# Optimization experiments

Measured on AMD Instinct MI355X. Metric: run time of the kernel, lower is better.

## Reference

```python
import jax, jax.numpy as jnp
import numpy as np

EPS = 0.01       # perturbation radius (constructor arg)
MEAN = 0.1307    # MNIST normalize constants from the 'else' branch
SIGMA = 0.3081


def _get_bound(v, eps):
    # torch get_bound detaches eps before taking |.| and summing
    r = jnp.sum(jnp.abs(jax.lax.stop_gradient(eps)), axis=-1)
    return v + r, v - r


def _relu_zono(v, eps):
    # v: [N], eps: [N, E]. Append one fresh (zero) error column, as the torch code does.
    n = v.shape[0]
    eps = jnp.concatenate([eps, jnp.zeros((n, 1), eps.dtype)], axis=-1)  # [N, E+1]
    u, l = _get_bound(v, eps)
    denom = u - l  # = 2*sum|eps| >= 0; guard against 0 for non-crossing rows
    # slopes are created as Parameters = u/(u-l) on the first pass (detached leaf)
    slope = jax.lax.stop_gradient(u / jnp.where(denom == 0, 1.0, denom))
    # at init slope == base = u/(u-l), so the slope <= base branch is taken
    term = (1.0 - slope) * u * 0.5
    crossing = (u > 0) & (l < 0)
    dead = u <= 0
    # torch uses slope.data * values.data for the linear part, + term (term carries grad)
    v_cross = jax.lax.stop_gradient(slope * v) + term
    v_new = jnp.where(dead, 0.0, jnp.where(crossing, v_cross, v))
    eps_cross = jnp.concatenate([slope[:, None] * eps[:, :-1], term[:, None]], axis=-1)
    eps_new = jnp.where(dead[:, None], 0.0, jnp.where(crossing[:, None], eps_cross, eps))
    return v_new, eps_new


def _forward(inputs, W1, b1, W2, b2, W3, b3):
    # initial zonotope build (faithful to source: values = u + l, radii = values - l = u)
    upper = jnp.minimum(inputs + EPS, 1.0)   # upper - relu(upper - 1)
    lower = jnp.maximum(inputs - EPS, 0.0)   # relu(lower)
    values = upper + lower
    eps = jnp.diag((values - lower).flatten())  # [D, D]
    # Normalize layer (the 'else' branch)
    values = (values - MEAN) / SIGMA
    eps = eps / SIGMA
    # Flatten
    v = values.flatten()
    # Linear -> ReLU -> Linear -> ReLU -> Linear
    v = W1 @ v + b1
    eps = W1 @ eps
    v, eps = _relu_zono(v, eps)
    v = W2 @ v + b2
    eps = W2 @ eps
    v, eps = _relu_zono(v, eps)
    v = W3 @ v + b3
    eps = W3 @ eps
    u, l = _get_bound(v, eps)
    return u, l


def setup_inputs() -> dict:
    key = jax.random.key(0)
    ks = jax.random.split(key, 7)
    D, H, O = 1024, 4096, 10
    inputs = jax.random.uniform(ks[0], (1, 1, 32, 32), jnp.float32)
    W1 = jax.random.normal(ks[1], (H, D), jnp.float32) / np.float32(np.sqrt(D))
    b1 = jax.random.normal(ks[2], (H,), jnp.float32) * 0.01
    W2 = jax.random.normal(ks[3], (H, H), jnp.float32) / np.float32(np.sqrt(H))
    b2 = jax.random.normal(ks[4], (H,), jnp.float32) * 0.01
    W3 = jax.random.normal(ks[5], (O, H), jnp.float32) / np.float32(np.sqrt(H))
    b3 = jax.random.normal(ks[6], (O,), jnp.float32) * 0.01
    return {"inputs": inputs, "W1": W1, "b1": b1, "W2": W2, "b2": b2, "W3": W3, "b3": b3}


def reference(inputs, W1, b1, W2, b2, W3, b3):
    return _forward(inputs, W1, b1, W2, b2, W3, b3)
```

## Files before the change

kernel.cpp:

```cpp
#include <hip/hip_runtime.h>
#include <math.h>

#define ZEPS  0.01f
#define ZMEAN 0.1307f
#define ZSIGMA 0.3081f

constexpr int D = 1024, H = 4096, O = 10;

using short8 = __attribute__((ext_vector_type(8))) short;
using f32x4  = __attribute__((ext_vector_type(4))) float;

__device__ inline unsigned short f2bf(float x) {
    unsigned int u = __float_as_uint(x);
    u += 0x7FFFu + ((u >> 16) & 1u);
    return (unsigned short)(u >> 16);
}

__device__ inline void gl_lds16(const void* g, void* l) {
    __builtin_amdgcn_global_load_lds(
        (const __attribute__((address_space(1))) unsigned int*)g,
        (__attribute__((address_space(3))) unsigned int*)l, 16, 0, 0);
}

__device__ inline void relu_params(float v, float r, float& vout, float& aout, float& tout) {
    float u = v + r, l = v - r;
    float denom = u - l;
    float slope = u / (denom == 0.f ? 1.f : denom);
    float term = (1.f - slope) * u * 0.5f;
    bool dead = (u <= 0.f);
    bool crossing = (u > 0.f) && (l < 0.f);
    vout = dead ? 0.f : (crossing ? (slope * v + term) : v);
    aout = dead ? 0.f : (crossing ? slope : 1.f);
    tout = (!dead && crossing) ? term : 0.f;
}

__global__ void k_setup(const float* __restrict__ x, float* __restrict__ values,
                        float* __restrict__ dcol, float* __restrict__ r3) {
    int j = blockIdx.x * blockDim.x + threadIdx.x;
    if (j < D) {
        float v = x[j];
        float up = fminf(v + ZEPS, 1.f);
        float lo = fmaxf(v - ZEPS, 0.f);
        values[j] = (up + lo - ZMEAN) / ZSIGMA;
        dcol[j]   = up / ZSIGMA;
    }
    if (blockIdx.x == 0 && threadIdx.x < 16) r3[threadIdx.x] = 0.f;
}

__global__ __launch_bounds__(256) void k_layer1(const float* __restrict__ W1, const float* __restrict__ b1,
                                                const float* __restrict__ values, const float* __restrict__ dcol,
                                                float* __restrict__ v1p, float* __restrict__ a1,
                                                float* __restrict__ t1) {
    int i = blockIdx.x, tid = threadIdx.x;
    const float* row = W1 + (size_t)i * D;
    float sv = 0.f, sr = 0.f;
    for (int j = tid; j < D; j += 256) {
        float w = row[j];
        sv += w * values[j];
        sr += fabsf(w) * dcol[j];
    }
    __shared__ float red1[256], red2[256];
    red1[tid] = sv; red2[tid] = sr;
    __syncthreads();
    for (int off = 128; off; off >>= 1) {
        if (tid < off) { red1[tid] += red1[tid + off]; red2[tid] += red2[tid + off]; }
        __syncthreads();
    }
    if (tid == 0) {
        float v = red1[0] + b1[i];
        relu_params(v, red2[0], v1p[i], a1[i], t1[i]);
    }
}

__global__ __launch_bounds__(256) void k_scaleT(const float* __restrict__ W1, const float* __restrict__ a1,
                                                const float* __restrict__ dcol,
                                                unsigned short* __restrict__ W1sT) {
    __shared__ float tile[32][33];
    int j0 = blockIdx.x * 32, k0 = blockIdx.y * 32;
    int r = threadIdx.x >> 3;
    int c = (threadIdx.x & 7) * 4;
    float4 w = *(const float4*)&W1[(size_t)(k0 + r) * D + j0 + c];
    float a = a1[k0 + r];
    tile[r][c + 0] = a * w.x * dcol[j0 + c + 0];
    tile[r][c + 1] = a * w.y * dcol[j0 + c + 1];
    tile[r][c + 2] = a * w.z * dcol[j0 + c + 2];
    tile[r][c + 3] = a * w.w * dcol[j0 + c + 3];
    __syncthreads();
    ushort4 o;
    o.x = f2bf(tile[c + 0][r]);
    o.y = f2bf(tile[c + 1][r]);
    o.z = f2bf(tile[c + 2][r]);
    o.w = f2bf(tile[c + 3][r]);
    *(ushort4*)&W1sT[(size_t)(j0 + r) * H + k0 + c] = o;
}

__global__ __launch_bounds__(256) void k_v2conv(const float* __restrict__ W2, const float* __restrict__ b2,
                                                const float* __restrict__ v1p, const float* __restrict__ t1,
                                                float* __restrict__ v2, float* __restrict__ t2col,
                                                unsigned short* __restrict__ W2b) {
    int i = blockIdx.x, tid = threadIdx.x;
    const float* row = W2 + (size_t)i * H;
    unsigned short* orow = W2b + (size_t)i * H;
    float sv = 0.f, st = 0.f;
    for (int k0 = tid * 4; k0 < H; k0 += 1024) {
        float4 w = *(const float4*)&row[k0];
        sv += w.x * v1p[k0] + w.y * v1p[k0 + 1] + w.z * v1p[k0 + 2] + w.w * v1p[k0 + 3];
        st += w.x * t1[k0] + w.y * t1[k0 + 1] + w.z * t1[k0 + 2] + w.w * t1[k0 + 3];
        ushort4 o;
        o.x = f2bf(w.x); o.y = f2bf(w.y); o.z = f2bf(w.z); o.w = f2bf(w.w);
        *(ushort4*)&orow[k0] = o;
    }
    __shared__ float red1[256], red2[256];
    red1[tid] = sv; red2[tid] = st;
    __syncthreads();
    for (int off = 128; off; off >>= 1) {
        if (tid < off) { red1[tid] += red1[tid + off]; red2[tid] += red2[tid + off]; }
        __syncthreads();
    }
    if (tid == 0) { v2[i] = red1[0] + b2[i]; t2col[i] = red2[0]; }
}

#define GBK 64
__global__ __launch_bounds__(256) void k_gemm_mfma(const unsigned short* __restrict__ A,
                                                   const unsigned short* __restrict__ B,
                                                   float* __restrict__ C) {
    const int N = D, K = H;
    __shared__ __align__(16) unsigned short As[128 * GBK];
    __shared__ __align__(16) unsigned short Bs[128 * GBK];
    int tid = threadIdx.x;
    int wave = tid >> 6, lane = tid & 63;
    int bm = blockIdx.y * 128, bn = blockIdx.x * 128;
    int kbeg = blockIdx.z * (K / 2), kend = kbeg + K / 2;
    float* Cz = C + (size_t)blockIdx.z * ((size_t)H * D);
    int wm = (wave >> 1) * 64, wn = (wave & 1) * 64;

    int sr = lane >> 3;
    int sc = lane & 7;
    int scp = sc ^ sr;
    int r15 = lane & 15, quad = lane >> 4, key = r15 & 7;

    f32x4 acc[4][4];
#pragma unroll
    for (int p = 0; p < 4; ++p)
#pragma unroll
        for (int q = 0; q < 4; ++q) acc[p][q] = (f32x4){0.f, 0.f, 0.f, 0.f};

    for (int k0 = kbeg; k0 < kend; k0 += GBK) {
#pragma unroll
        for (int g = 0; g < 4; ++g) {
            int row = wave * 32 + g * 8;
            gl_lds16(&A[(size_t)(bm + row + sr) * K + k0 + scp * 8], &As[row * GBK]);
            gl_lds16(&B[(size_t)(bn + row + sr) * K + k0 + scp * 8], &Bs[row * GBK]);
        }
        __syncthreads();
#pragma unroll
        for (int kk = 0; kk < 2; ++kk) {
            short8 af[4], bf[4];
#pragma unroll
            for (int mt = 0; mt < 4; ++mt)
                af[mt] = *(const short8*)&As[(wm + mt * 16 + r15) * GBK + (((kk * 4 + quad) ^ key)) * 8];
#pragma unroll
            for (int nt = 0; nt < 4; ++nt)
                bf[nt] = *(const short8*)&Bs[(wn + nt * 16 + r15) * GBK + (((kk * 4 + quad) ^ key)) * 8];
#pragma unroll
            for (int mt = 0; mt < 4; ++mt)
#pragma unroll
                for (int nt = 0; nt < 4; ++nt)
                    acc[mt][nt] = __builtin_amdgcn_mfma_f32_16x16x32_bf16(af[mt], bf[nt], acc[mt][nt], 0, 0, 0);
        }
        __syncthreads();
    }

#pragma unroll
    for (int mt = 0; mt < 4; ++mt) {
        int gr = bm + wm + mt * 16 + quad * 4;
#pragma unroll
        for (int nt = 0; nt < 4; ++nt) {
            int gc = bn + wn + nt * 16 + r15;
            Cz[(size_t)(gr + 0) * N + gc] = acc[mt][nt][0];
            Cz[(size_t)(gr + 1) * N + gc] = acc[mt][nt][1];
            Cz[(size_t)(gr + 2) * N + gc] = acc[mt][nt][2];
            Cz[(size_t)(gr + 3) * N + gc] = acc[mt][nt][3];
        }
    }
}

__global__ __launch_bounds__(256) void k_relu2(const float* __restrict__ e1, const float* __restrict__ e2,
                                               const float* __restrict__ t2col,
                                               const float* __restrict__ v2, float* __restrict__ v2p,
                                               float* __restrict__ a2, float* __restrict__ t2) {
    int i = blockIdx.x, tid = threadIdx.x;
    float4 a = ((const float4*)(e1 + (size_t)i * D))[tid];
    float4 b = ((const float4*)(e2 + (size_t)i * D))[tid];
    float s = fabsf(a.x + b.x) + fabsf(a.y + b.y) + fabsf(a.z + b.z) + fabsf(a.w + b.w);
    __shared__ float red[256];
    red[tid] = s;
    __syncthreads();
    for (int off = 128; off; off >>= 1) {
        if (tid < off) red[tid] += red[tid + off];
        __syncthreads();
    }
    if (tid == 0) {
        float r = red[0] + fabsf(t2col[i]);
        relu_params(v2[i], r, v2p[i], a2[i], t2[i]);
    }
}

__global__ void k_w3s(const float* __restrict__ W3, const float* __restrict__ a2,
                      float* __restrict__ w3s) {
    int i = blockIdx.x * blockDim.x + threadIdx.x;
    if (i < H) {
        float a = a2[i];
#pragma unroll
        for (int o = 0; o < O; ++o) w3s[(size_t)i * O + o] = W3[(size_t)o * H + i] * a;
    }
}

__global__ __launch_bounds__(256) void k_eps3a(const float* __restrict__ e1, const float* __restrict__ e2,
                                               const float* __restrict__ w3s,
                                               float* __restrict__ pbuf) {
    int jb = blockIdx.x, ib = blockIdx.y;
    int c = threadIdx.x & 63, s = threadIdx.x >> 6;
    int j = jb * 64 + c;
    int i0 = ib * 128 + s * 32;
    float acc[O];
#pragma unroll
    for (int o = 0; o < O; ++o) acc[o] = 0.f;
    for (int ii = 0; ii < 32; ++ii) {
        int i = i0 + ii;
        float e = e1[(size_t)i * D + j] + e2[(size_t)i * D + j];
        const float* w = &w3s[(size_t)i * O];
#pragma unroll
        for (int o = 0; o < O; ++o) acc[o] += w[o] * e;
    }
    __shared__ float sm[4][64][O];
#pragma unroll
    for (int o = 0; o < O; ++o) sm[s][c][o] = acc[o];
    __syncthreads();
    for (int idx = threadIdx.x; idx < 64 * O; idx += 256) {
        int o = idx >> 6, cc = idx & 63;
        float t = sm[0][cc][o] + sm[1][cc][o] + sm[2][cc][o] + sm[3][cc][o];
        pbuf[((size_t)ib * O + o) * D + jb * 64 + cc] = t;
    }
}

__global__ __launch_bounds__(256) void k_eps3b(const float* __restrict__ pbuf, float* __restrict__ r3) {
    int o = blockIdx.x, tid = threadIdx.x;
    float s = 0.f;
    for (int j = tid; j < D; j += 256) {
        float t = 0.f;
#pragma unroll
        for (int ib = 0; ib < 32; ++ib) t += pbuf[((size_t)ib * O + o) * D + j];
        s += fabsf(t);
    }
    __shared__ float red[256];
    red[tid] = s;
    __syncthreads();
    for (int off = 128; off; off >>= 1) {
        if (tid < off) red[tid] += red[tid + off];
        __syncthreads();
    }
    if (tid == 0) r3[o] = red[0];
}

__global__ __launch_bounds__(256) void k_final(const float* __restrict__ W3, const float* __restrict__ b3,
                                               const float* __restrict__ v2p, const float* __restrict__ a2,
                                               const float* __restrict__ t2col, const float* __restrict__ t2,
                                               const float* __restrict__ r3, float* __restrict__ out) {
    int o = blockIdx.x, tid = threadIdx.x;
    const float* row = W3 + (size_t)o * H;
    float sv = 0.f, s1 = 0.f, s2 = 0.f;
    for (int i = tid; i < H; i += 256) {
        float w = row[i];
        sv += w * v2p[i];
        s1 += w * a2[i] * t2col[i];
        s2 += w * t2[i];
    }
    __shared__ float ra[256], rb[256], rc[256];
    ra[tid] = sv; rb[tid] = s1; rc[tid] = s2;
    __syncthreads();
    for (int off = 128; off; off >>= 1) {
        if (tid < off) { ra[tid] += ra[tid + off]; rb[tid] += rb[tid + off]; rc[tid] += rc[tid + off]; }
        __syncthreads();
    }
    if (tid == 0) {
        float v3 = ra[0] + b3[o];
        float rr = r3[o] + fabsf(rb[0]) + fabsf(rc[0]);
        out[o] = v3 + rr;
        out[O + o] = v3 - rr;
    }
}

extern "C" void kernel_launch(void* const* d_in, const int* in_sizes, int n_in,
                              void* d_out, int out_size, void* d_ws, size_t ws_size,
                              hipStream_t stream) {
    const float* x  = (const float*)d_in[0];
    const float* W1 = (const float*)d_in[1];
    const float* b1 = (const float*)d_in[2];
    const float* W2 = (const float*)d_in[3];
    const float* b2 = (const float*)d_in[4];
    const float* W3 = (const float*)d_in[5];
    const float* b3 = (const float*)d_in[6];
    float* out = (float*)d_out;

    float* p = (float*)d_ws;
    float* values = p; p += D;
    float* dcol   = p; p += D;
    float* v1p    = p; p += H;
    float* a1     = p; p += H;
    float* t1     = p; p += H;
    float* v2     = p; p += H;
    float* t2col  = p; p += H;
    float* v2p    = p; p += H;
    float* a2     = p; p += H;
    float* t2     = p; p += H;
    float* r3     = p; p += 16;
    p += 16;
    float* w3s    = p; p += H * O + 8;
    float* pbuf   = p; p += 32 * O * D;
    float* eps2   = p; p += (size_t)2 * H * D;
    unsigned short* W2b  = (unsigned short*)p;
    unsigned short* W1sT = W2b + (size_t)H * H;
    float* eps2b = eps2 + (size_t)H * D;

    k_setup<<<dim3((D + 255) / 256), 256, 0, stream>>>(x, values, dcol, r3);
    k_layer1<<<H, 256, 0, stream>>>(W1, b1, values, dcol, v1p, a1, t1);
    k_scaleT<<<dim3(D / 32, H / 32), 256, 0, stream>>>(W1, a1, dcol, W1sT);
    k_v2conv<<<H, 256, 0, stream>>>(W2, b2, v1p, t1, v2, t2col, W2b);
    k_gemm_mfma<<<dim3(D / 128, H / 128, 2), 256, 0, stream>>>(W2b, W1sT, eps2);
    k_relu2<<<H, 256, 0, stream>>>(eps2, eps2b, t2col, v2, v2p, a2, t2);
    k_w3s<<<(H + 255) / 256, 256, 0, stream>>>(W3, a2, w3s);
    k_eps3a<<<dim3(D / 64, 32), 256, 0, stream>>>(eps2, eps2b, w3s, pbuf);
    k_eps3b<<<O, 256, 0, stream>>>(pbuf, r3);
    k_final<<<O, 256, 0, stream>>>(W3, b3, v2p, a2, t2col, t2, r3, out);
}
```

Baseline: 228.3 us.

## Fuse setup, w3s and eps3b kernels; remap GEMM blocks; vectorize eps3a

Removes three small kernels by recomputing the input transform inline in layer1/scaleT, folding the W3 scaling into relu2, and merging the final eps3 reduction into k_final. The GEMM grid is flattened to 1D with a remapping that places both K-halves and neighbouring tiles on adjacent block IDs, likely for cache locality across XCDs. k_eps3a now processes four columns per thread with float4 loads, and the pbuf layout is transposed so k_final reads it contiguously. The goal is fewer launches and better memory access, at the cost of a heavier 16-way shared reduction in eps3a and a k_final that does more serial work in only 10 blocks.

```diff
diff --git a/kernel.cpp b/kernel.cpp
--- a/kernel.cpp
+++ b/kernel.cpp
@@ -20,6 +20,15 @@
     __builtin_amdgcn_global_load_lds(
         (const __attribute__((address_space(1))) unsigned int*)g,
         (__attribute__((address_space(3))) unsigned int*)l, 16, 0, 0);
+}
+
+__device__ inline float zval(float xv) {
+    float up = fminf(xv + ZEPS, 1.f);
+    float lo = fmaxf(xv - ZEPS, 0.f);
+    return (up + lo - ZMEAN) / ZSIGMA;
+}
+__device__ inline float zdia(float xv) {
+    return fminf(xv + ZEPS, 1.f) / ZSIGMA;
 }
 
 __device__ inline void relu_params(float v, float r, float& vout, float& aout, float& tout) {
@@ -34,21 +43,8 @@
     tout = (!dead && crossing) ? term : 0.f;
 }
 
-__global__ void k_setup(const float* __restrict__ x, float* __restrict__ values,
-                        float* __restrict__ dcol, float* __restrict__ r3) {
-    int j = blockIdx.x * blockDim.x + threadIdx.x;
-    if (j < D) {
-        float v = x[j];
-        float up = fminf(v + ZEPS, 1.f);
-        float lo = fmaxf(v - ZEPS, 0.f);
-        values[j] = (up + lo - ZMEAN) / ZSIGMA;
-        dcol[j]   = up / ZSIGMA;
-    }
-    if (blockIdx.x == 0 && threadIdx.x < 16) r3[threadIdx.x] = 0.f;
-}
-
 __global__ __launch_bounds__(256) void k_layer1(const float* __restrict__ W1, const float* __restrict__ b1,
-                                                const float* __restrict__ values, const float* __restrict__ dcol,
+                                                const float* __restrict__ x,
                                                 float* __restrict__ v1p, float* __restrict__ a1,
                                                 float* __restrict__ t1) {
     int i = blockIdx.x, tid = threadIdx.x;
@@ -56,8 +52,9 @@
     float sv = 0.f, sr = 0.f;
     for (int j = tid; j < D; j += 256) {
         float w = row[j];
-        sv += w * values[j];
-        sr += fabsf(w) * dcol[j];
+        float xv = x[j];
+        sv += w * zval(xv);
+        sr += fabsf(w) * zdia(xv);
     }
     __shared__ float red1[256], red2[256];
     red1[tid] = sv; red2[tid] = sr;
@@ -73,18 +70,19 @@
 }
 
 __global__ __launch_bounds__(256) void k_scaleT(const float* __restrict__ W1, const float* __restrict__ a1,
-                                                const float* __restrict__ dcol,
+                                                const float* __restrict__ x,
                                                 unsigned short* __restrict__ W1sT) {
     __shared__ float tile[32][33];
     int j0 = blockIdx.x * 32, k0 = blockIdx.y * 32;
     int r = threadIdx.x >> 3;
     int c = (threadIdx.x & 7) * 4;
     float4 w = *(const float4*)&W1[(size_t)(k0 + r) * D + j0 + c];
+    float4 xx = *(const float4*)&x[j0 + c];
     float a = a1[k0 + r];
-    tile[r][c + 0] = a * w.x * dcol[j0 + c + 0];
-    tile[r][c + 1] = a * w.y * dcol[j0 + c + 1];
-    tile[r][c + 2] = a * w.z * dcol[j0 + c + 2];
-    tile[r][c + 3] = a * w.w * dcol[j0 + c + 3];
+    tile[r][c + 0] = a * w.x * zdia(xx.x);
+    tile[r][c + 1] = a * w.y * zdia(xx.y);
+    tile[r][c + 2] = a * w.z * zdia(xx.z);
+    tile[r][c + 3] = a * w.w * zdia(xx.w);
     __syncthreads();
     ushort4 o;
     o.x = f2bf(tile[c + 0][r]);
@@ -127,11 +125,16 @@
     const int N = D, K = H;
     __shared__ __align__(16) unsigned short As[128 * GBK];
     __shared__ __align__(16) unsigned short Bs[128 * GBK];
+    int b = blockIdx.x;
+    int u = b & 7, v = b >> 3;
+    int z = u >> 2;
+    int y = (u & 3) * 8 + (v >> 3);
+    int xb = v & 7;
     int tid = threadIdx.x;
     int wave = tid >> 6, lane = tid & 63;
-    int bm = blockIdx.y * 128, bn = blockIdx.x * 128;
-    int kbeg = blockIdx.z * (K / 2), kend = kbeg + K / 2;
-    float* Cz = C + (size_t)blockIdx.z * ((size_t)H * D);
+    int bm = y * 128, bn = xb * 128;
+    int kbeg = z * (K / 2), kend = kbeg + K / 2;
+    float* Cz = C + (size_t)z * ((size_t)H * D);
     int wm = (wave >> 1) * 64, wn = (wave & 1) * 64;
 
     int sr = lane >> 3;
@@ -187,13 +190,16 @@
 
 __global__ __launch_bounds__(256) void k_relu2(const float* __restrict__ e1, const float* __restrict__ e2,
                                                const float* __restrict__ t2col,
-                                               const float* __restrict__ v2, float* __restrict__ v2p,
-                                               float* __restrict__ a2, float* __restrict__ t2) {
+                                               const float* __restrict__ v2, const float* __restrict__ W3,
+                                               float* __restrict__ v2p,
+                                               float* __restrict__ a2, float* __restrict__ t2,
+                                               float* __restrict__ w3s) {
     int i = blockIdx.x, tid = threadIdx.x;
     float4 a = ((const float4*)(e1 + (size_t)i * D))[tid];
     float4 b = ((const float4*)(e2 + (size_t)i * D))[tid];
     float s = fabsf(a.x + b.x) + fabsf(a.y + b.y) + fabsf(a.z + b.z) + fabsf(a.w + b.w);
     __shared__ float red[256];
+    __shared__ float s_a2;
     red[tid] = s;
     __syncthreads();
     for (int off = 128; off; off >>= 1) {
@@ -202,72 +208,67 @@
     }
     if (tid == 0) {
         float r = red[0] + fabsf(t2col[i]);
-        relu_params(v2[i], r, v2p[i], a2[i], t2[i]);
-    }
-}
-
-__global__ void k_w3s(const float* __restrict__ W3, const float* __restrict__ a2,
-                      float* __restrict__ w3s) {
-    int i = blockIdx.x * blockDim.x + threadIdx.x;
-    if (i < H) {
-        float a = a2[i];
-#pragma unroll
-        for (int o = 0; o < O; ++o) w3s[(size_t)i * O + o] = W3[(size_t)o * H + i] * a;
-    }
+        float vo, ao, to;
+        relu_params(v2[i], r, vo, ao, to);
+        v2p[i] = vo; a2[i] = ao; t2[i] = to;
+        s_a2 = ao;
+    }
+    __syncthreads();
+    if (tid < O) w3s[(size_t)i * O + tid] = W3[(size_t)tid * H + i] * s_a2;
 }
 
 __global__ __launch_bounds__(256) void k_eps3a(const float* __restrict__ e1, const float* __restrict__ e2,
                                                const float* __restrict__ w3s,
                                                float* __restrict__ pbuf) {
     int jb = blockIdx.x, ib = blockIdx.y;
-    int c = threadIdx.x & 63, s = threadIdx.x >> 6;
-    int j = jb * 64 + c;
-    int i0 = ib * 128 + s * 32;
-    float acc[O];
-#pragma unroll
-    for (int o = 0; o < O; ++o) acc[o] = 0.f;
-    for (int ii = 0; ii < 32; ++ii) {
+    int jj = threadIdx.x & 15, s = threadIdx.x >> 4;
+    int j = jb * 64 + jj * 4;
+    int i0 = ib * 128 + s * 8;
+    float acc[4][O];
+#pragma unroll
+    for (int c = 0; c < 4; ++c)
+#pragma unroll
+        for (int o = 0; o < O; ++o) acc[c][o] = 0.f;
+    for (int ii = 0; ii < 8; ++ii) {
         int i = i0 + ii;
-        float e = e1[(size_t)i * D + j] + e2[(size_t)i * D + j];
+        float4 a = *(const float4*)&e1[(size_t)i * D + j];
+        float4 b = *(const float4*)&e2[(size_t)i * D + j];
+        float e0 = a.x + b.x, ee1 = a.y + b.y, ee2 = a.z + b.z, ee3 = a.w + b.w;
         const float* w = &w3s[(size_t)i * O];
 #pragma unroll
-        for (int o = 0; o < O; ++o) acc[o] += w[o] * e;
-    }
-    __shared__ float sm[4][64][O];
-#pragma unroll
-    for (int o = 0; o < O; ++o) sm[s][c][o] = acc[o];
+        for (int o = 0; o < O; ++o) {
+            float wo = w[o];
+            acc[0][o] += wo * e0; acc[1][o] += wo * ee1;
+            acc[2][o] += wo * ee2; acc[3][o] += wo * ee3;
+        }
+    }
+    __shared__ float sm[16][64][O];
+#pragma unroll
+    for (int c = 0; c < 4; ++c)
+#pragma unroll
+        for (int o = 0; o < O; ++o) sm[s][jj * 4 + c][o] = acc[c][o];
     __syncthreads();
     for (int idx = threadIdx.x; idx < 64 * O; idx += 256) {
-        int o = idx >> 6, cc = idx & 63;
-        float t = sm[0][cc][o] + sm[1][cc][o] + sm[2][cc][o] + sm[3][cc][o];
-        pbuf[((size_t)ib * O + o) * D + jb * 64 + cc] = t;
-    }
-}
-
-__global__ __launch_bounds__(256) void k_eps3b(const float* __restrict__ pbuf, float* __restrict__ r3) {
-    int o = blockIdx.x, tid = threadIdx.x;
-    float s = 0.f;
-    for (int j = tid; j < D; j += 256) {
+        int col = idx / O, o = idx % O;
         float t = 0.f;
 #pragma unroll
-        for (int ib = 0; ib < 32; ++ib) t += pbuf[((size_t)ib * O + o) * D + j];
-        s += fabsf(t);
-    }
-    __shared__ float red[256];
-    red[tid] = s;
-    __syncthreads();
-    for (int off = 128; off; off >>= 1) {
-        if (tid < off) red[tid] += red[tid + off];
-        __syncthreads();
-    }
-    if (tid == 0) r3[o] = red[0];
+        for (int ss = 0; ss < 16; ++ss) t += sm[ss][col][o];
+        pbuf[((size_t)o * 32 + ib) * D + jb * 64 + col] = t;
+    }
 }
 
 __global__ __launch_bounds__(256) void k_final(const float* __restrict__ W3, const float* __restrict__ b3,
                                                const float* __restrict__ v2p, const float* __restrict__ a2,
                                                const float* __restrict__ t2col, const float* __restrict__ t2,
-                                               const float* __restrict__ r3, float* __restrict__ out) {
+                                               const float* __restrict__ pbuf, float* __restrict__ out) {
     int o = blockIdx.x, tid = threadIdx.x;
+    float s3 = 0.f;
+    for (int j = tid; j < D; j += 256) {
+        float t = 0.f;
+#pragma unroll
+        for (int ib = 0; ib < 32; ++ib) t += pbuf[((size_t)o * 32 + ib) * D + j];
+        s3 += fabsf(t);
+    }
     const float* row = W3 + (size_t)o * H;
     float sv = 0.f, s1 = 0.f, s2 = 0.f;
     for (int i = tid; i < H; i += 256) {
@@ -276,16 +277,19 @@
         s1 += w * a2[i] * t2col[i];
         s2 += w * t2[i];
     }
-    __shared__ float ra[256], rb[256], rc[256];
-    ra[tid] = sv; rb[tid] = s1; rc[tid] = s2;
+    __shared__ float ra[256], rb[256], rc[256], rd[256];
+    ra[tid] = sv; rb[tid] = s1; rc[tid] = s2; rd[tid] = s3;
     __syncthreads();
     for (int off = 128; off; off >>= 1) {
-        if (tid < off) { ra[tid] += ra[tid + off]; rb[tid] += rb[tid + off]; rc[tid] += rc[tid + off]; }
+        if (tid < off) {
+            ra[tid] += ra[tid + off]; rb[tid] += rb[tid + off];
+            rc[tid] += rc[tid + off]; rd[tid] += rd[tid + off];
+        }
         __syncthreads();
     }
     if (tid == 0) {
         float v3 = ra[0] + b3[o];
-        float rr = r3[o] + fabsf(rb[0]) + fabsf(rc[0]);
+        float rr = rd[0] + fabsf(rb[0]) + fabsf(rc[0]);
         out[o] = v3 + rr;
         out[O + o] = v3 - rr;
     }
@@ -304,8 +308,6 @@
     float* out = (float*)d_out;
 
     float* p = (float*)d_ws;
-    float* values = p; p += D;
-    float* dcol   = p; p += D;
     float* v1p    = p; p += H;
     float* a1     = p; p += H;
     float* t1     = p; p += H;
@@ -314,8 +316,6 @@
     float* v2p    = p; p += H;
     float* a2     = p; p += H;
     float* t2     = p; p += H;
-    float* r3     = p; p += 16;
-    p += 16;
     float* w3s    = p; p += H * O + 8;
     float* pbuf   = p; p += 32 * O * D;
     float* eps2   = p; p += (size_t)2 * H * D;
@@ -323,14 +323,11 @@
     unsigned short* W1sT = W2b + (size_t)H * H;
     float* eps2b = eps2 + (size_t)H * D;
 
-    k_setup<<<dim3((D + 255) / 256), 256, 0, stream>>>(x, values, dcol, r3);
-    k_layer1<<<H, 256, 0, stream>>>(W1, b1, values, dcol, v1p, a1, t1);
-    k_scaleT<<<dim3(D / 32, H / 32), 256, 0, stream>>>(W1, a1, dcol, W1sT);
+    k_layer1<<<H, 256, 0, stream>>>(W1, b1, x, v1p, a1, t1);
+    k_scaleT<<<dim3(D / 32, H / 32), 256, 0, stream>>>(W1, a1, x, W1sT);
     k_v2conv<<<H, 256, 0, stream>>>(W2, b2, v1p, t1, v2, t2col, W2b);
-    k_gemm_mfma<<<dim3(D / 128, H / 128, 2), 256, 0, stream>>>(W2b, W1sT, eps2);
-    k_relu2<<<H, 256, 0, stream>>>(eps2, eps2b, t2col, v2, v2p, a2, t2);
-    k_w3s<<<(H + 255) / 256, 256, 0, stream>>>(W3, a2, w3s);
+    k_gemm_mfma<<<512, 256, 0, stream>>>(W2b, W1sT, eps2);
+    k_relu2<<<H, 256, 0, stream>>>(eps2, eps2b, t2col, v2, W3, v2p, a2, t2, w3s);
     k_eps3a<<<dim3(D / 64, 32), 256, 0, stream>>>(eps2, eps2b, w3s, pbuf);
-    k_eps3b<<<O, 256, 0, stream>>>(pbuf, r3);
-    k_final<<<O, 256, 0, stream>>>(W3, b3, v2p, a2, t2col, t2, r3, out);
-}
+    k_final<<<O, 256, 0, stream>>>(W3, b3, v2p, a2, t2col, t2, pbuf, out);
+}
```

Result: faster. 221.6 us (-2.9%).
